# Kernel tuning notes

Measured on AMD Instinct MI355X. Metric: run time of the kernel, lower is better.

## Reference

```python
import jax, jax.numpy as jnp
import numpy as np

B, N, D, W = 4, 4096, 256, 7
K = 2 * W + 1  # 15 taps: positions [i-2w, ..., i]
H = 4 * D
EPS = 1e-5


def layer_norm(x, g, b):
    mu = jnp.mean(x, axis=-1, keepdims=True)
    var = jnp.mean(jnp.square(x - mu), axis=-1, keepdims=True)
    return (x - mu) * jax.lax.rsqrt(var + EPS) * g + b


def setup_inputs() -> dict:
    key = jax.random.key(0)
    ks = jax.random.split(key, 8)
    s = 0.02
    return {
        "x": jax.random.normal(ks[0], (B, N, D), dtype=jnp.float32),
        # w_mix[k] is the DxD block of the (K*D -> D) Linear acting on offset k-2w
        "w_mix": (jax.random.normal(ks[1], (K, D, D), dtype=jnp.float32) * s),
        "b_mix": jnp.zeros((D,), dtype=jnp.float32),
        "g1": jnp.ones((D,), jnp.float32) + 0.1 * jax.random.normal(ks[2], (D,), jnp.float32),
        "b1": 0.1 * jax.random.normal(ks[3], (D,), jnp.float32),
        "w_ff1": jax.random.normal(ks[4], (D, H), dtype=jnp.float32) * s,
        "b_ff1": jnp.zeros((H,), dtype=jnp.float32),
        "w_ff2": jax.random.normal(ks[5], (H, D), dtype=jnp.float32) * s,
        "b_ff2": jnp.zeros((D,), dtype=jnp.float32),
        "g2": jnp.ones((D,), jnp.float32) + 0.1 * jax.random.normal(ks[6], (D,), jnp.float32),
        "b2": 0.1 * jax.random.normal(ks[7], (D,), jnp.float32),
    }


def reference(x, w_mix, b_mix, g1, b1, w_ff1, b_ff1, w_ff2, b_ff2, g2, b2):
    # Causal windowed concat + Linear == causal 1D conv with kernel K=2w+1.
    # torch feats chunk k holds x[i - 2w + k]; conv tap k with left pad 2w
    # sees exactly x[i - 2w + k], so kernel = mix weight reshaped (K, D, D).
    mix = jax.lax.conv_general_dilated(
        x, w_mix, window_strides=(1,), padding=[(2 * W, 0)],
        dimension_numbers=("NWC", "WIO", "NWC"),
    ) + b_mix  # [B, N, D]
    # Dropout is identity in eval mode (reference baseline).
    h = layer_norm(x + mix, g1, b1)
    ff = jnp.dot(jax.nn.gelu(jnp.dot(h, w_ff1) + b_ff1, approximate=False), w_ff2) + b_ff2
    return layer_norm(h + ff, g2, b2)
```

## Files before the change

kernel.cpp:

```cpp
#include <hip/hip_runtime.h>
#include <cstdint>

#define DD     256
#define HH     1024
#define NNSEQ  4096
#define KDIM   3840
#define NSTEPS 120
#define MT     64
#define XROWS  78
#define XPITCH 264
#define EPSLN  1e-5f

typedef unsigned short u16;
typedef __attribute__((ext_vector_type(8))) short short8;
typedef __attribute__((ext_vector_type(4))) float f32x4;

#define MFMA(a, b, c) __builtin_amdgcn_mfma_f32_16x16x32_bf16(a, b, c, 0, 0, 0)

__device__ __forceinline__ u16 f2bf(float f) {
  unsigned u = __float_as_uint(f);
  u += 0x7FFF + ((u >> 16) & 1);
  return (u16)(u >> 16);
}
__device__ __forceinline__ float bf2f(u16 s) { return __uint_as_float(((unsigned)s) << 16); }

__global__ __launch_bounds__(256) void k_prep(
    const float* __restrict__ wmix, const float* __restrict__ wff1,
    const float* __restrict__ wff2, u16* __restrict__ wpk,
    u16* __restrict__ w1pk, u16* __restrict__ w2pk)
{
  __shared__ float t[32][257];
  const int b = blockIdx.x, tid = threadIdx.x;

  u16* dst;
  if (b < 120) {
    dst = wpk + (size_t)b * 8192;
    for (int r = 0; r < 32; ++r)
      t[r][tid] = wmix[(size_t)(b * 32 + r) * 256 + tid];
  } else if (b < 152) {
    const int u = b - 120, c = u >> 3, s = u & 7;
    dst = w1pk + (size_t)u * 8192;
    for (int r = 0; r < 32; ++r)
      t[r][tid] = wff1[(size_t)(s * 32 + r) * 1024 + c * 256 + tid];
  } else {
    const int u = b - 152, c = u >> 3, s = u & 7;
    dst = w2pk + (size_t)u * 8192;
    for (int r = 0; r < 32; ++r)
      t[r][tid] = wff2[(size_t)(c * 256 + s * 32 + r) * 256 + tid];
  }
  __syncthreads();

  const int l = tid & 63, q = l >> 4, cl = l & 15;
#pragma unroll
  for (int f = 0; f < 4; ++f) {
    const int fi = f * 4 + (tid >> 6);
    const int n = fi * 16 + cl;
    uint4 pk;
    unsigned* p = (unsigned*)&pk;
#pragma unroll
    for (int jj = 0; jj < 4; ++jj)
      p[jj] = (unsigned)f2bf(t[q * 8 + jj * 2][n]) | ((unsigned)f2bf(t[q * 8 + jj * 2 + 1][n]) << 16);
    *(uint4*)&dst[(size_t)fi * 512 + l * 8] = pk;
  }
}

__global__ __launch_bounds__(512, 2) void k_fused(
    const float* __restrict__ x, const u16* __restrict__ wpk,
    const float* __restrict__ bmix, const float* __restrict__ g1,
    const float* __restrict__ b1, const u16* __restrict__ w1pk,
    const float* __restrict__ bf1, const u16* __restrict__ w2pk,
    const float* __restrict__ bf2, const float* __restrict__ g2,
    const float* __restrict__ b2, float* __restrict__ out)
{
  __shared__ u16 smA[XROWS * XPITCH];
  __shared__ u16 asb[64 * XPITCH];
  __shared__ float redS[4][64], redS2[4][64];
  __shared__ float muL[64], invL[64];

  const int tid = threadIdx.x;
  const int wv = tid >> 6, l = tid & 63, q = l >> 4, cl = l & 15;
  const int mg = wv >> 2, ng = wv & 3;
  const long tok0 = (long)blockIdx.x * MT;
  const int n0 = (int)(tok0 & (NNSEQ - 1));

  {
    const int cslot = (tid & 63) * 4;
    for (int r = tid >> 6; r < XROWS; r += 8) {
      const int nloc = n0 - 14 + r;
      float4 v = make_float4(0.f, 0.f, 0.f, 0.f);
      if (nloc >= 0) v = *(const float4*)&x[(tok0 - 14 + r) * DD + cslot];
      uint2 pk;
      pk.x = (unsigned)f2bf(v.x) | ((unsigned)f2bf(v.y) << 16);
      pk.y = (unsigned)f2bf(v.z) | ((unsigned)f2bf(v.w) << 16);
      *(uint2*)&smA[r * XPITCH + cslot] = pk;
    }
  }
  __syncthreads();

  f32x4 acc[2][4];
#pragma unroll
  for (int nt = 0; nt < 4; ++nt) {
    const float bm = bmix[ng * 64 + nt * 16 + cl];
#pragma unroll
    for (int mt = 0; mt < 2; ++mt) acc[mt][nt] = (f32x4){bm, bm, bm, bm};
  }

  const u16* bbase = wpk + (size_t)ng * 2048 + (size_t)l * 8;

#define LOAD_A(dst, s_)                                                        \
  {                                                                            \
    const int xrow = (s_) >> 3, c0 = ((s_) & 7) * 32;                          \
    _Pragma("unroll")                                                          \
    for (int mt = 0; mt < 2; ++mt)                                             \
      dst[mt] = *(const short8*)&smA[(xrow + mg * 32 + mt * 16 + cl) * XPITCH + c0 + q * 8]; \
  }
#define LOAD_B(dst, s_)                                                        \
  {                                                                            \
    const u16* bp = bbase + (size_t)(s_) * 8192;                               \
    _Pragma("unroll")                                                          \
    for (int nt = 0; nt < 4; ++nt)                                             \
      dst[nt] = *(const short8*)(bp + nt * 512);                               \
  }

  {
    short8 af[3][2], bfr[3][4];
    LOAD_A(af[0], 0) LOAD_B(bfr[0], 0)
    LOAD_A(af[1], 1) LOAD_B(bfr[1], 1)
    LOAD_A(af[2], 2) LOAD_B(bfr[2], 2)

#pragma unroll 3
    for (int s = 0; s < NSTEPS; ++s) {
      const int cur = s % 3;
#pragma unroll
      for (int mt = 0; mt < 2; ++mt)
#pragma unroll
        for (int nt = 0; nt < 4; ++nt)
          acc[mt][nt] = MFMA(af[cur][mt], bfr[cur][nt], acc[mt][nt]);
      if (s + 3 < NSTEPS) {
        LOAD_A(af[cur], s + 3)
        LOAD_B(bfr[cur], s + 3)
      }
    }
  }
#undef LOAD_A
#undef LOAD_B

#pragma unroll
  for (int mt = 0; mt < 2; ++mt)
#pragma unroll
    for (int nt = 0; nt < 4; ++nt) {
      const int col = ng * 64 + nt * 16 + cl;
#pragma unroll
      for (int reg = 0; reg < 4; ++reg) {
        const int row = mg * 32 + mt * 16 + q * 4 + reg;
        acc[mt][nt][reg] += x[(tok0 + row) * DD + col];
      }
    }

  {
    float ps[2][4], ps2[2][4];
#pragma unroll
    for (int mt = 0; mt < 2; ++mt)
#pragma unroll
      for (int reg = 0; reg < 4; ++reg) {
        float s = 0.f, s2 = 0.f;
#pragma unroll
        for (int nt = 0; nt < 4; ++nt) { const float y = acc[mt][nt][reg]; s += y; s2 += y * y; }
#pragma unroll
        for (int off = 1; off < 16; off <<= 1) { s += __shfl_xor(s, off, 64); s2 += __shfl_xor(s2, off, 64); }
        ps[mt][reg] = s; ps2[mt][reg] = s2;
      }
    if (cl == 0) {
#pragma unroll
      for (int mt = 0; mt < 2; ++mt)
#pragma unroll
        for (int reg = 0; reg < 4; ++reg) {
          const int row = mg * 32 + mt * 16 + q * 4 + reg;
          redS[ng][row] = ps[mt][reg]; redS2[ng][row] = ps2[mt][reg];
        }
    }
  }
  __syncthreads();
  if (tid < 64) {
    const float s  = redS[0][tid] + redS[1][tid] + redS[2][tid] + redS[3][tid];
    const float s2 = redS2[0][tid] + redS2[1][tid] + redS2[2][tid] + redS2[3][tid];
    const float mu = s * (1.f / DD);
    const float var = s2 * (1.f / DD) - mu * mu;
    muL[tid] = mu; invL[tid] = rsqrtf(var + EPSLN);
  }
  __syncthreads();

#pragma unroll
  for (int nt = 0; nt < 4; ++nt) {
    const int col = ng * 64 + nt * 16 + cl;
    const float gv = g1[col], bv = b1[col];
#pragma unroll
    for (int mt = 0; mt < 2; ++mt)
#pragma unroll
      for (int reg = 0; reg < 4; ++reg) {
        const int row = mg * 32 + mt * 16 + q * 4 + reg;
        const float hv = (acc[mt][nt][reg] - muL[row]) * invL[row] * gv + bv;
        smA[row * XPITCH + col] = f2bf(hv);
      }
  }
  __syncthreads();

  f32x4 acc2[2][4];
#pragma unroll
  for (int nt = 0; nt < 4; ++nt) {
    const float bv = bf2[ng * 64 + nt * 16 + cl];
#pragma unroll
    for (int mt = 0; mt < 2; ++mt) acc2[mt][nt] = (f32x4){bv, bv, bv, bv};
  }

  for (int c = 0; c < 4; ++c) {
    f32x4 acc1[2][4];
#pragma unroll
    for (int nt = 0; nt < 4; ++nt) {
      const float bv = bf1[c * 256 + ng * 64 + nt * 16 + cl];
#pragma unroll
      for (int mt = 0; mt < 2; ++mt) acc1[mt][nt] = (f32x4){bv, bv, bv, bv};
    }
#pragma unroll
    for (int s = 0; s < 8; ++s) {
      short8 a[2], b[4];
#pragma unroll
      for (int mt = 0; mt < 2; ++mt)
        a[mt] = *(const short8*)&smA[(mg * 32 + mt * 16 + cl) * XPITCH + s * 32 + q * 8];
      const u16* bp = w1pk + (size_t)(c * 8 + s) * 8192 + ng * 2048 + (size_t)l * 8;
#pragma unroll
      for (int nt = 0; nt < 4; ++nt)
        b[nt] = *(const short8*)(bp + nt * 512);
#pragma unroll
      for (int mt = 0; mt < 2; ++mt)
#pragma unroll
        for (int nt = 0; nt < 4; ++nt)
          acc1[mt][nt] = MFMA(a[mt], b[nt], acc1[mt][nt]);
    }
#pragma unroll
    for (int mt = 0; mt < 2; ++mt)
#pragma unroll
      for (int nt = 0; nt < 4; ++nt)
#pragma unroll
        for (int reg = 0; reg < 4; ++reg) {
          const float v = acc1[mt][nt][reg];
          const float g = 0.5f * v * (1.f + erff(v * 0.70710678118654752f));
          asb[(mg * 32 + mt * 16 + q * 4 + reg) * XPITCH + ng * 64 + nt * 16 + cl] = f2bf(g);
        }
    __syncthreads();
#pragma unroll
    for (int s = 0; s < 8; ++s) {
      short8 a[2], b[4];
#pragma unroll
      for (int mt = 0; mt < 2; ++mt)
        a[mt] = *(const short8*)&asb[(mg * 32 + mt * 16 + cl) * XPITCH + s * 32 + q * 8];
      const u16* bp = w2pk + (size_t)(c * 8 + s) * 8192 + ng * 2048 + (size_t)l * 8;
#pragma unroll
      for (int nt = 0; nt < 4; ++nt)
        b[nt] = *(const short8*)(bp + nt * 512);
#pragma unroll
      for (int mt = 0; mt < 2; ++mt)
#pragma unroll
        for (int nt = 0; nt < 4; ++nt)
          acc2[mt][nt] = MFMA(a[mt], b[nt], acc2[mt][nt]);
    }
    __syncthreads();
  }

#pragma unroll
  for (int mt = 0; mt < 2; ++mt)
#pragma unroll
    for (int nt = 0; nt < 4; ++nt) {
      const int col = ng * 64 + nt * 16 + cl;
#pragma unroll
      for (int reg = 0; reg < 4; ++reg) {
        const int row = mg * 32 + mt * 16 + q * 4 + reg;
        acc2[mt][nt][reg] += bf2f(smA[row * XPITCH + col]);
      }
    }

  {
    float ps[2][4], ps2[2][4];
#pragma unroll
    for (int mt = 0; mt < 2; ++mt)
#pragma unroll
      for (int reg = 0; reg < 4; ++reg) {
        float s = 0.f, s2 = 0.f;
#pragma unroll
        for (int nt = 0; nt < 4; ++nt) { const float y = acc2[mt][nt][reg]; s += y; s2 += y * y; }
#pragma unroll
        for (int off = 1; off < 16; off <<= 1) { s += __shfl_xor(s, off, 64); s2 += __shfl_xor(s2, off, 64); }
        ps[mt][reg] = s; ps2[mt][reg] = s2;
      }
    if (cl == 0) {
#pragma unroll
      for (int mt = 0; mt < 2; ++mt)
#pragma unroll
        for (int reg = 0; reg < 4; ++reg) {
          const int row = mg * 32 + mt * 16 + q * 4 + reg;
          redS[ng][row] = ps[mt][reg]; redS2[ng][row] = ps2[mt][reg];
        }
    }
  }
  __syncthreads();
  if (tid < 64) {
    const float s  = redS[0][tid] + redS[1][tid] + redS[2][tid] + redS[3][tid];
    const float s2 = redS2[0][tid] + redS2[1][tid] + redS2[2][tid] + redS2[3][tid];
    const float mu = s * (1.f / DD);
    const float var = s2 * (1.f / DD) - mu * mu;
    muL[tid] = mu; invL[tid] = rsqrtf(var + EPSLN);
  }
  __syncthreads();

#pragma unroll
  for (int nt = 0; nt < 4; ++nt) {
    const int col = ng * 64 + nt * 16 + cl;
    const float gv = g2[col], bv = b2[col];
#pragma unroll
    for (int mt = 0; mt < 2; ++mt)
#pragma unroll
      for (int reg = 0; reg < 4; ++reg) {
        const int row = mg * 32 + mt * 16 + q * 4 + reg;
        out[(tok0 + row) * DD + col] = (acc2[mt][nt][reg] - muL[row]) * invL[row] * gv + bv;
      }
  }
}

extern "C" void kernel_launch(void* const* d_in, const int* in_sizes, int n_in,
                              void* d_out, int out_size, void* d_ws, size_t ws_size,
                              hipStream_t stream) {
  const float* x    = (const float*)d_in[0];
  const float* wmix = (const float*)d_in[1];
  const float* bmix = (const float*)d_in[2];
  const float* g1   = (const float*)d_in[3];
  const float* b1   = (const float*)d_in[4];
  const float* wff1 = (const float*)d_in[5];
  const float* bff1 = (const float*)d_in[6];
  const float* wff2 = (const float*)d_in[7];
  const float* bff2 = (const float*)d_in[8];
  const float* g2   = (const float*)d_in[9];
  const float* b2   = (const float*)d_in[10];
  float* out = (float*)d_out;

  u16* wpk  = (u16*)d_ws;
  u16* w1pk = wpk + 983040;
  u16* w2pk = w1pk + 262144;

  k_prep<<<184, 256, 0, stream>>>(wmix, wff1, wff2, wpk, w1pk, w2pk);

  const int R = 4 * NNSEQ;
  k_fused<<<R / MT, 512, 0, stream>>>(x, wpk, bmix, g1, b1,
                                      w1pk, bff1, w2pk, bff2, g2, b2, out);
}
```

Baseline: 168.1 us.

## Split fused kernel into conv and FFN kernels with split-K wave groups

```diff
diff --git a/kernel.cpp b/kernel.cpp
--- a/kernel.cpp
+++ b/kernel.cpp
@@ -5,10 +5,11 @@
 #define HH     1024
 #define NNSEQ  4096
 #define KDIM   3840
-#define NSTEPS 120
 #define MT     64
 #define XROWS  78
 #define XPITCH 264
+#define APITCH 520
+#define FPITCH 260
 #define EPSLN  1e-5f
 
 typedef unsigned short u16;
@@ -38,15 +39,15 @@
     for (int r = 0; r < 32; ++r)
       t[r][tid] = wmix[(size_t)(b * 32 + r) * 256 + tid];
   } else if (b < 152) {
-    const int u = b - 120, c = u >> 3, s = u & 7;
+    const int u = b - 120, c2 = u >> 3, s = u & 7;
     dst = w1pk + (size_t)u * 8192;
     for (int r = 0; r < 32; ++r)
-      t[r][tid] = wff1[(size_t)(s * 32 + r) * 1024 + c * 256 + tid];
+      t[r][tid] = wff1[(size_t)(s * 32 + r) * 1024 + c2 * 256 + tid];
   } else {
-    const int u = b - 152, c = u >> 3, s = u & 7;
+    const int u = b - 152, c2 = u >> 3, s = u & 7;
     dst = w2pk + (size_t)u * 8192;
     for (int r = 0; r < 32; ++r)
-      t[r][tid] = wff2[(size_t)(c * 256 + s * 32 + r) * 256 + tid];
+      t[r][tid] = wff2[(size_t)(c2 * 256 + s * 32 + r) * 256 + tid];
   }
   __syncthreads();
 
@@ -64,23 +65,17 @@
   }
 }
 
-__global__ __launch_bounds__(512, 2) void k_fused(
+__global__ __launch_bounds__(512) void k_conv(
     const float* __restrict__ x, const u16* __restrict__ wpk,
-    const float* __restrict__ bmix, const float* __restrict__ g1,
-    const float* __restrict__ b1, const u16* __restrict__ w1pk,
-    const float* __restrict__ bf1, const u16* __restrict__ w2pk,
-    const float* __restrict__ bf2, const float* __restrict__ g2,
-    const float* __restrict__ b2, float* __restrict__ out)
+    const float* __restrict__ bmix, u16* __restrict__ yb)
 {
-  __shared__ u16 smA[XROWS * XPITCH];
-  __shared__ u16 asb[64 * XPITCH];
-  __shared__ float redS[4][64], redS2[4][64];
-  __shared__ float muL[64], invL[64];
+  __shared__ u16 xs[XROWS * XPITCH];
 
   const int tid = threadIdx.x;
   const int wv = tid >> 6, l = tid & 63, q = l >> 4, cl = l & 15;
   const int mg = wv >> 2, ng = wv & 3;
-  const long tok0 = (long)blockIdx.x * MT;
+  const int mtile = blockIdx.x >> 2, nb = blockIdx.x & 3;
+  const long tok0 = (long)mtile * MT;
   const int n0 = (int)(tok0 & (NNSEQ - 1));
 
   {
@@ -92,90 +87,248 @@
       uint2 pk;
       pk.x = (unsigned)f2bf(v.x) | ((unsigned)f2bf(v.y) << 16);
       pk.y = (unsigned)f2bf(v.z) | ((unsigned)f2bf(v.w) << 16);
-      *(uint2*)&smA[r * XPITCH + cslot] = pk;
-    }
-  }
-  __syncthreads();
-
-  f32x4 acc[2][4];
-#pragma unroll
-  for (int nt = 0; nt < 4; ++nt) {
-    const float bm = bmix[ng * 64 + nt * 16 + cl];
-#pragma unroll
-    for (int mt = 0; mt < 2; ++mt) acc[mt][nt] = (f32x4){bm, bm, bm, bm};
-  }
-
-  const u16* bbase = wpk + (size_t)ng * 2048 + (size_t)l * 8;
-
-#define LOAD_A(dst, s_)                                                        \
-  {                                                                            \
-    const int xrow = (s_) >> 3, c0 = ((s_) & 7) * 32;                          \
-    _Pragma("unroll")                                                          \
-    for (int mt = 0; mt < 2; ++mt)                                             \
-      dst[mt] = *(const short8*)&smA[(xrow + mg * 32 + mt * 16 + cl) * XPITCH + c0 + q * 8]; \
-  }
-#define LOAD_B(dst, s_)                                                        \
-  {                                                                            \
-    const u16* bp = bbase + (size_t)(s_) * 8192;                               \
-    _Pragma("unroll")                                                          \
-    for (int nt = 0; nt < 4; ++nt)                                             \
-      dst[nt] = *(const short8*)(bp + nt * 512);                               \
-  }
-
-  {
-    short8 af[3][2], bfr[3][4];
+      *(uint2*)&xs[r * XPITCH + cslot] = pk;
+    }
+  }
+  __syncthreads();
+
+  f32x4 acc[4];
+  {
+    const float bm = (mg == 0) ? bmix[nb * 64 + ng * 16 + cl] : 0.f;
+#pragma unroll
+    for (int mt = 0; mt < 4; ++mt) acc[mt] = (f32x4){bm, bm, bm, bm};
+  }
+
+  const u16* bbase = wpk + (size_t)(mg * 60) * 8192 + (size_t)(nb * 4 + ng) * 512 + (size_t)l * 8;
+
+#define LOAD_A(dst, s_)                                                         \
+  {                                                                             \
+    const int ks = mg * 60 + (s_);                                              \
+    const int xrow = ks >> 3, c0 = (ks & 7) * 32;                               \
+    _Pragma("unroll")                                                           \
+    for (int mt = 0; mt < 4; ++mt)                                              \
+      dst[mt] = *(const short8*)&xs[(xrow + mt * 16 + cl) * XPITCH + c0 + q * 8]; \
+  }
+#define LOAD_B(dst, s_) dst = *(const short8*)(bbase + (size_t)(s_) * 8192);
+
+  {
+    short8 af[4][4], bfr[4];
     LOAD_A(af[0], 0) LOAD_B(bfr[0], 0)
     LOAD_A(af[1], 1) LOAD_B(bfr[1], 1)
     LOAD_A(af[2], 2) LOAD_B(bfr[2], 2)
-
-#pragma unroll 3
-    for (int s = 0; s < NSTEPS; ++s) {
-      const int cur = s % 3;
-#pragma unroll
-      for (int mt = 0; mt < 2; ++mt)
-#pragma unroll
-        for (int nt = 0; nt < 4; ++nt)
-          acc[mt][nt] = MFMA(af[cur][mt], bfr[cur][nt], acc[mt][nt]);
-      if (s + 3 < NSTEPS) {
-        LOAD_A(af[cur], s + 3)
-        LOAD_B(bfr[cur], s + 3)
+    LOAD_A(af[3], 3) LOAD_B(bfr[3], 3)
+
+#pragma unroll 4
+    for (int s = 0; s < 60; ++s) {
+      const int cur = s & 3;
+#pragma unroll
+      for (int mt = 0; mt < 4; ++mt)
+        acc[mt] = MFMA(af[cur][mt], bfr[cur], acc[mt]);
+      if (s + 4 < 60) {
+        LOAD_A(af[cur], s + 4)
+        LOAD_B(bfr[cur], s + 4)
       }
     }
   }
 #undef LOAD_A
 #undef LOAD_B
 
-#pragma unroll
-  for (int mt = 0; mt < 2; ++mt)
+  __syncthreads();
+  float* rbuf = (float*)xs;
+  if (mg == 1) {
+#pragma unroll
+    for (int mt = 0; mt < 4; ++mt)
+#pragma unroll
+      for (int reg = 0; reg < 4; ++reg)
+        rbuf[(mt * 16 + q * 4 + reg) * 65 + ng * 16 + cl] = acc[mt][reg];
+  }
+  __syncthreads();
+
+  if (mg == 0) {
+#pragma unroll
+    for (int mt = 0; mt < 4; ++mt)
+#pragma unroll
+      for (int reg = 0; reg < 4; ++reg) {
+        const int row = mt * 16 + q * 4 + reg;
+        const int col = nb * 64 + ng * 16 + cl;
+        const float y = acc[mt][reg] + rbuf[row * 65 + ng * 16 + cl]
+                      + x[(tok0 + row) * DD + col];
+        yb[(tok0 + row) * DD + col] = f2bf(y);
+      }
+  }
+}
+
+__global__ __launch_bounds__(512) void k_ffn(
+    const u16* __restrict__ yb, const float* __restrict__ g1,
+    const float* __restrict__ b1, const u16* __restrict__ w1pk,
+    const float* __restrict__ bf1, const u16* __restrict__ w2pk,
+    const float* __restrict__ bf2, const float* __restrict__ g2,
+    const float* __restrict__ b2, float* __restrict__ out)
+{
+  __shared__ u16 hs[64 * XPITCH];
+  __shared__ u16 asb[64 * APITCH];
+  __shared__ float redS[4][64], redS2[4][64];
+  __shared__ float muL[64], invL[64];
+
+  const int tid = threadIdx.x;
+  const int wv = tid >> 6, l = tid & 63, q = l >> 4, cl = l & 15;
+  const int mg = wv >> 2, ng = wv & 3;
+  const long tok0 = (long)blockIdx.x * MT;
+
+  {
+    const int chunk = tid & 31;
+#pragma unroll
+    for (int i = 0; i < 4; ++i) {
+      const int row = (tid >> 5) + i * 16;
+      *(uint4*)&hs[row * XPITCH + chunk * 8] = *(const uint4*)&yb[(tok0 + row) * DD + chunk * 8];
+    }
+  }
+  __syncthreads();
+
+  {
+    const int row = tid >> 3, seg = tid & 7;
+    uint4 v[4];
+#pragma unroll
+    for (int i = 0; i < 4; ++i)
+      v[i] = *(const uint4*)&hs[row * XPITCH + seg * 32 + i * 8];
+    float yv[32];
+#pragma unroll
+    for (int i = 0; i < 4; ++i) {
+      const unsigned* w = (const unsigned*)&v[i];
+#pragma unroll
+      for (int j = 0; j < 4; ++j) {
+        yv[i * 8 + j * 2]     = __uint_as_float(w[j] << 16);
+        yv[i * 8 + j * 2 + 1] = __uint_as_float(w[j] & 0xffff0000u);
+      }
+    }
+    float s = 0.f, s2 = 0.f;
+#pragma unroll
+    for (int k = 0; k < 32; ++k) { s += yv[k]; s2 += yv[k] * yv[k]; }
+#pragma unroll
+    for (int off = 1; off < 8; off <<= 1) { s += __shfl_xor(s, off, 64); s2 += __shfl_xor(s2, off, 64); }
+    const float mu  = s * (1.f / DD);
+    const float var = s2 * (1.f / DD) - mu * mu;
+    const float inv = rsqrtf(var + EPSLN);
+#pragma unroll
+    for (int i = 0; i < 4; ++i) {
+      const float4 gv0 = *(const float4*)&g1[seg * 32 + i * 8];
+      const float4 gv1 = *(const float4*)&g1[seg * 32 + i * 8 + 4];
+      const float4 bv0 = *(const float4*)&b1[seg * 32 + i * 8];
+      const float4 bv1 = *(const float4*)&b1[seg * 32 + i * 8 + 4];
+      const float g[8] = {gv0.x, gv0.y, gv0.z, gv0.w, gv1.x, gv1.y, gv1.z, gv1.w};
+      const float bb[8] = {bv0.x, bv0.y, bv0.z, bv0.w, bv1.x, bv1.y, bv1.z, bv1.w};
+      uint4 pk;
+      unsigned* p = (unsigned*)&pk;
+#pragma unroll
+      for (int j = 0; j < 4; ++j) {
+        const float h0 = (yv[i * 8 + j * 2]     - mu) * inv * g[j * 2]     + bb[j * 2];
+        const float h1 = (yv[i * 8 + j * 2 + 1] - mu) * inv * g[j * 2 + 1] + bb[j * 2 + 1];
+        p[j] = (unsigned)f2bf(h0) | ((unsigned)f2bf(h1) << 16);
+      }
+      *(uint4*)&hs[row * XPITCH + seg * 32 + i * 8] = pk;
+    }
+  }
+  __syncthreads();
+
+  f32x4 acc2[4][4];
+#pragma unroll
+  for (int nt = 0; nt < 4; ++nt) {
+    const float bv = (mg == 0) ? bf2[ng * 64 + nt * 16 + cl] : 0.f;
+#pragma unroll
+    for (int mt = 0; mt < 4; ++mt) acc2[mt][nt] = (f32x4){bv, bv, bv, bv};
+  }
+
+  for (int c = 0; c < 2; ++c) {
+    f32x4 acc1[4][4];
 #pragma unroll
     for (int nt = 0; nt < 4; ++nt) {
-      const int col = ng * 64 + nt * 16 + cl;
+      const float bv = bf1[c * 512 + wv * 64 + nt * 16 + cl];
+#pragma unroll
+      for (int mt = 0; mt < 4; ++mt) acc1[mt][nt] = (f32x4){bv, bv, bv, bv};
+    }
+#pragma unroll
+    for (int s = 0; s < 8; ++s) {
+      short8 a[4], b[4];
+#pragma unroll
+      for (int mt = 0; mt < 4; ++mt)
+        a[mt] = *(const short8*)&hs[(mt * 16 + cl) * XPITCH + s * 32 + q * 8];
+      const u16* bp = w1pk + (size_t)((c * 2 + mg) * 8 + s) * 8192 + (size_t)(ng * 4) * 512 + (size_t)l * 8;
+#pragma unroll
+      for (int nt = 0; nt < 4; ++nt)
+        b[nt] = *(const short8*)(bp + nt * 512);
+#pragma unroll
+      for (int mt = 0; mt < 4; ++mt)
+#pragma unroll
+        for (int nt = 0; nt < 4; ++nt)
+          acc1[mt][nt] = MFMA(a[mt], b[nt], acc1[mt][nt]);
+    }
+#pragma unroll
+    for (int mt = 0; mt < 4; ++mt)
+#pragma unroll
+      for (int nt = 0; nt < 4; ++nt)
+#pragma unroll
+        for (int reg = 0; reg < 4; ++reg) {
+          const float v = acc1[mt][nt][reg];
+          const float g = 0.5f * v * (1.f + erff(v * 0.70710678118654752f));
+          asb[(mt * 16 + q * 4 + reg) * APITCH + wv * 64 + nt * 16 + cl] = f2bf(g);
+        }
+    __syncthreads();
+#pragma unroll
+    for (int s = 0; s < 8; ++s) {
+      short8 a[4], b[4];
+#pragma unroll
+      for (int mt = 0; mt < 4; ++mt)
+        a[mt] = *(const short8*)&asb[(mt * 16 + cl) * APITCH + mg * 256 + s * 32 + q * 8];
+      const u16* bp = w2pk + (size_t)((c * 2 + mg) * 8 + s) * 8192 + (size_t)(ng * 4) * 512 + (size_t)l * 8;
+#pragma unroll
+      for (int nt = 0; nt < 4; ++nt)
+        b[nt] = *(const short8*)(bp + nt * 512);
+#pragma unroll
+      for (int mt = 0; mt < 4; ++mt)
+#pragma unroll
+        for (int nt = 0; nt < 4; ++nt)
+          acc2[mt][nt] = MFMA(a[mt], b[nt], acc2[mt][nt]);
+    }
+    __syncthreads();
+  }
+
+  float* fbuf = (float*)asb;
+  if (mg == 1) {
+#pragma unroll
+    for (int mt = 0; mt < 4; ++mt)
+#pragma unroll
+      for (int nt = 0; nt < 4; ++nt)
+#pragma unroll
+        for (int reg = 0; reg < 4; ++reg)
+          fbuf[(mt * 16 + q * 4 + reg) * FPITCH + ng * 64 + nt * 16 + cl] = acc2[mt][nt][reg];
+  }
+  __syncthreads();
+
+  if (mg == 0) {
+    float ps[4][4], ps2[4][4];
+#pragma unroll
+    for (int mt = 0; mt < 4; ++mt)
 #pragma unroll
       for (int reg = 0; reg < 4; ++reg) {
-        const int row = mg * 32 + mt * 16 + q * 4 + reg;
-        acc[mt][nt][reg] += x[(tok0 + row) * DD + col];
-      }
-    }
-
-  {
-    float ps[2][4], ps2[2][4];
-#pragma unroll
-    for (int mt = 0; mt < 2; ++mt)
-#pragma unroll
-      for (int reg = 0; reg < 4; ++reg) {
+        const int row = mt * 16 + q * 4 + reg;
         float s = 0.f, s2 = 0.f;
 #pragma unroll
-        for (int nt = 0; nt < 4; ++nt) { const float y = acc[mt][nt][reg]; s += y; s2 += y * y; }
+        for (int nt = 0; nt < 4; ++nt) {
+          const int col = ng * 64 + nt * 16 + cl;
+          float y = acc2[mt][nt][reg] + fbuf[row * FPITCH + col] + bf2f(hs[row * XPITCH + col]);
+          acc2[mt][nt][reg] = y;
+          s += y; s2 += y * y;
+        }
 #pragma unroll
         for (int off = 1; off < 16; off <<= 1) { s += __shfl_xor(s, off, 64); s2 += __shfl_xor(s2, off, 64); }
         ps[mt][reg] = s; ps2[mt][reg] = s2;
       }
     if (cl == 0) {
 #pragma unroll
-      for (int mt = 0; mt < 2; ++mt)
+      for (int mt = 0; mt < 4; ++mt)
 #pragma unroll
         for (int reg = 0; reg < 4; ++reg) {
-          const int row = mg * 32 + mt * 16 + q * 4 + reg;
+          const int row = mt * 16 + q * 4 + reg;
           redS[ng][row] = ps[mt][reg]; redS2[ng][row] = ps2[mt][reg];
         }
     }
@@ -190,139 +343,19 @@
   }
   __syncthreads();
 
-#pragma unroll
-  for (int nt = 0; nt < 4; ++nt) {
-    const int col = ng * 64 + nt * 16 + cl;
-    const float gv = g1[col], bv = b1[col];
-#pragma unroll
-    for (int mt = 0; mt < 2; ++mt)
-#pragma unroll
-      for (int reg = 0; reg < 4; ++reg) {
-        const int row = mg * 32 + mt * 16 + q * 4 + reg;
-        const float hv = (acc[mt][nt][reg] - muL[row]) * invL[row] * gv + bv;
-        smA[row * XPITCH + col] = f2bf(hv);
-      }
-  }
-  __syncthreads();
-
-  f32x4 acc2[2][4];
-#pragma unroll
-  for (int nt = 0; nt < 4; ++nt) {
-    const float bv = bf2[ng * 64 + nt * 16 + cl];
-#pragma unroll
-    for (int mt = 0; mt < 2; ++mt) acc2[mt][nt] = (f32x4){bv, bv, bv, bv};
-  }
-
-  for (int c = 0; c < 4; ++c) {
-    f32x4 acc1[2][4];
-#pragma unroll
-    for (int nt = 0; nt < 4; ++nt) {
-      const float bv = bf1[c * 256 + ng * 64 + nt * 16 + cl];
-#pragma unroll
-      for (int mt = 0; mt < 2; ++mt) acc1[mt][nt] = (f32x4){bv, bv, bv, bv};
-    }
-#pragma unroll
-    for (int s = 0; s < 8; ++s) {
-      short8 a[2], b[4];
-#pragma unroll
-      for (int mt = 0; mt < 2; ++mt)
-        a[mt] = *(const short8*)&smA[(mg * 32 + mt * 16 + cl) * XPITCH + s * 32 + q * 8];
-      const u16* bp = w1pk + (size_t)(c * 8 + s) * 8192 + ng * 2048 + (size_t)l * 8;
-#pragma unroll
-      for (int nt = 0; nt < 4; ++nt)
-        b[nt] = *(const short8*)(bp + nt * 512);
-#pragma unroll
-      for (int mt = 0; mt < 2; ++mt)
-#pragma unroll
-        for (int nt = 0; nt < 4; ++nt)
-          acc1[mt][nt] = MFMA(a[mt], b[nt], acc1[mt][nt]);
-    }
-#pragma unroll
-    for (int mt = 0; mt < 2; ++mt)
-#pragma unroll
-      for (int nt = 0; nt < 4; ++nt)
-#pragma unroll
-        for (int reg = 0; reg < 4; ++reg) {
-          const float v = acc1[mt][nt][reg];
-          const float g = 0.5f * v * (1.f + erff(v * 0.70710678118654752f));
-          asb[(mg * 32 + mt * 16 + q * 4 + reg) * XPITCH + ng * 64 + nt * 16 + cl] = f2bf(g);
-        }
-    __syncthreads();
-#pragma unroll
-    for (int s = 0; s < 8; ++s) {
-      short8 a[2], b[4];
-#pragma unroll
-      for (int mt = 0; mt < 2; ++mt)
-        a[mt] = *(const short8*)&asb[(mg * 32 + mt * 16 + cl) * XPITCH + s * 32 + q * 8];
-      const u16* bp = w2pk + (size_t)(c * 8 + s) * 8192 + ng * 2048 + (size_t)l * 8;
-#pragma unroll
-      for (int nt = 0; nt < 4; ++nt)
-        b[nt] = *(const short8*)(bp + nt * 512);
-#pragma unroll
-      for (int mt = 0; mt < 2; ++mt)
-#pragma unroll
-        for (int nt = 0; nt < 4; ++nt)
-          acc2[mt][nt] = MFMA(a[mt], b[nt], acc2[mt][nt]);
-    }
-    __syncthreads();
-  }
-
-#pragma unroll
-  for (int mt = 0; mt < 2; ++mt)
+  if (mg == 0) {
 #pragma unroll
     for (int nt = 0; nt < 4; ++nt) {
       const int col = ng * 64 + nt * 16 + cl;
-#pragma unroll
-      for (int reg = 0; reg < 4; ++reg) {
-        const int row = mg * 32 + mt * 16 + q * 4 + reg;
-        acc2[mt][nt][reg] += bf2f(smA[row * XPITCH + col]);
-      }
-    }
-
-  {
-    float ps[2][4], ps2[2][4];
-#pragma unroll
-    for (int mt = 0; mt < 2; ++mt)
-#pragma unroll
-      for (int reg = 0; reg < 4; ++reg) {
-        float s = 0.f, s2 = 0.f;
-#pragma unroll
-        for (int nt = 0; nt < 4; ++nt) { const float y = acc2[mt][nt][reg]; s += y; s2 += y * y; }
-#pragma unroll
-        for (int off = 1; off < 16; off <<= 1) { s += __shfl_xor(s, off, 64); s2 += __shfl_xor(s2, off, 64); }
-        ps[mt][reg] = s; ps2[mt][reg] = s2;
-      }
-    if (cl == 0) {
-#pragma unroll
-      for (int mt = 0; mt < 2; ++mt)
+      const float gv = g2[col], bv = b2[col];
+#pragma unroll
+      for (int mt = 0; mt < 4; ++mt)
 #pragma unroll
         for (int reg = 0; reg < 4; ++reg) {
-          const int row = mg * 32 + mt * 16 + q * 4 + reg;
-          redS[ng][row] = ps[mt][reg]; redS2[ng][row] = ps2[mt][reg];
+          const int row = mt * 16 + q * 4 + reg;
+          out[(tok0 + row) * DD + col] = (acc2[mt][nt][reg] - muL[row]) * invL[row] * gv + bv;
         }
     }
-  }
-  __syncthreads();
-  if (tid < 64) {
-    const float s  = redS[0][tid] + redS[1][tid] + redS[2][tid] + redS[3][tid];
-    const float s2 = redS2[0][tid] + redS2[1][tid] + redS2[2][tid] + redS2[3][tid];
-    const float mu = s * (1.f / DD);
-    const float var = s2 * (1.f / DD) - mu * mu;
-    muL[tid] = mu; invL[tid] = rsqrtf(var + EPSLN);
-  }
-  __syncthreads();
-
-#pragma unroll
-  for (int nt = 0; nt < 4; ++nt) {
-    const int col = ng * 64 + nt * 16 + cl;
-    const float gv = g2[col], bv = b2[col];
-#pragma unroll
-    for (int mt = 0; mt < 2; ++mt)
-#pragma unroll
-      for (int reg = 0; reg < 4; ++reg) {
-        const int row = mg * 32 + mt * 16 + q * 4 + reg;
-        out[(tok0 + row) * DD + col] = (acc2[mt][nt][reg] - muL[row]) * invL[row] * gv + bv;
-      }
   }
 }
 
@@ -345,10 +378,10 @@
   u16* wpk  = (u16*)d_ws;
   u16* w1pk = wpk + 983040;
   u16* w2pk = w1pk + 262144;
+  u16* yb   = w2pk + 262144;
 
   k_prep<<<184, 256, 0, stream>>>(wmix, wff1, wff2, wpk, w1pk, w2pk);
 
-  const int R = 4 * NNSEQ;
-  k_fused<<<R / MT, 512, 0, stream>>>(x, wpk, bmix, g1, b1,
-                                      w1pk, bff1, w2pk, bff2, g2, b2, out);
-}
+  k_conv<<<1024, 512, 0, stream>>>(x, wpk, bmix, yb);
+  k_ffn <<<256, 512, 0, stream>>>(yb, g1, b1, w1pk, bff1, w2pk, bff2, g2, b2, out);
+}
```

New measurement: 165.6 us. No clear change (-1.5%).

## Split conv GEMM K-dimension across wave groups with LDS reduction

Applied to the files above, without the earlier changes.

```diff
diff --git a/kernel.cpp b/kernel.cpp
--- a/kernel.cpp
+++ b/kernel.cpp
@@ -5,10 +5,10 @@
 #define HH     1024
 #define NNSEQ  4096
 #define KDIM   3840
-#define NSTEPS 120
 #define MT     64
 #define XROWS  78
 #define XPITCH 264
+#define SLOTP  260
 #define EPSLN  1e-5f
 
 typedef unsigned short u16;
@@ -38,15 +38,15 @@
     for (int r = 0; r < 32; ++r)
       t[r][tid] = wmix[(size_t)(b * 32 + r) * 256 + tid];
   } else if (b < 152) {
-    const int u = b - 120, c = u >> 3, s = u & 7;
+    const int u = b - 120, c2 = u >> 3, s = u & 7;
     dst = w1pk + (size_t)u * 8192;
     for (int r = 0; r < 32; ++r)
-      t[r][tid] = wff1[(size_t)(s * 32 + r) * 1024 + c * 256 + tid];
+      t[r][tid] = wff1[(size_t)(s * 32 + r) * 1024 + c2 * 256 + tid];
   } else {
-    const int u = b - 152, c = u >> 3, s = u & 7;
+    const int u = b - 152, c2 = u >> 3, s = u & 7;
     dst = w2pk + (size_t)u * 8192;
     for (int r = 0; r < 32; ++r)
-      t[r][tid] = wff2[(size_t)(c * 256 + s * 32 + r) * 256 + tid];
+      t[r][tid] = wff2[(size_t)(c2 * 256 + s * 32 + r) * 256 + tid];
   }
   __syncthreads();
 
@@ -64,7 +64,7 @@
   }
 }
 
-__global__ __launch_bounds__(512, 2) void k_fused(
+__global__ __launch_bounds__(512) void k_fused(
     const float* __restrict__ x, const u16* __restrict__ wpk,
     const float* __restrict__ bmix, const float* __restrict__ g1,
     const float* __restrict__ b1, const u16* __restrict__ w1pk,
@@ -72,8 +72,8 @@
     const float* __restrict__ bf2, const float* __restrict__ g2,
     const float* __restrict__ b2, float* __restrict__ out)
 {
-  __shared__ u16 smA[XROWS * XPITCH];
-  __shared__ u16 asb[64 * XPITCH];
+  __shared__ u16 bufA[XROWS * XPITCH];
+  __shared__ float bufB[64 * SLOTP];
   __shared__ float redS[4][64], redS2[4][64];
   __shared__ float muL[64], invL[64];
 
@@ -92,51 +92,52 @@
       uint2 pk;
       pk.x = (unsigned)f2bf(v.x) | ((unsigned)f2bf(v.y) << 16);
       pk.y = (unsigned)f2bf(v.z) | ((unsigned)f2bf(v.w) << 16);
-      *(uint2*)&smA[r * XPITCH + cslot] = pk;
-    }
-  }
-  __syncthreads();
-
-  f32x4 acc[2][4];
+      *(uint2*)&bufA[r * XPITCH + cslot] = pk;
+    }
+  }
+  __syncthreads();
+
+  f32x4 acc[4][4];
 #pragma unroll
   for (int nt = 0; nt < 4; ++nt) {
-    const float bm = bmix[ng * 64 + nt * 16 + cl];
-#pragma unroll
-    for (int mt = 0; mt < 2; ++mt) acc[mt][nt] = (f32x4){bm, bm, bm, bm};
-  }
-
-  const u16* bbase = wpk + (size_t)ng * 2048 + (size_t)l * 8;
-
-#define LOAD_A(dst, s_)                                                        \
-  {                                                                            \
-    const int xrow = (s_) >> 3, c0 = ((s_) & 7) * 32;                          \
-    _Pragma("unroll")                                                          \
-    for (int mt = 0; mt < 2; ++mt)                                             \
-      dst[mt] = *(const short8*)&smA[(xrow + mg * 32 + mt * 16 + cl) * XPITCH + c0 + q * 8]; \
-  }
-#define LOAD_B(dst, s_)                                                        \
-  {                                                                            \
-    const u16* bp = bbase + (size_t)(s_) * 8192;                               \
-    _Pragma("unroll")                                                          \
-    for (int nt = 0; nt < 4; ++nt)                                             \
-      dst[nt] = *(const short8*)(bp + nt * 512);                               \
+    const float bm = (mg == 0) ? bmix[ng * 64 + nt * 16 + cl] : 0.f;
+#pragma unroll
+    for (int mt = 0; mt < 4; ++mt) acc[mt][nt] = (f32x4){bm, bm, bm, bm};
+  }
+
+  const u16* bbase = wpk + (size_t)(mg * 60) * 8192 + (size_t)(ng * 4) * 512 + (size_t)l * 8;
+
+#define LOAD_A(dst, s_)                                                         \
+  {                                                                             \
+    const int ks = mg * 60 + (s_);                                              \
+    const int xrow = ks >> 3, c0 = (ks & 7) * 32;                               \
+    _Pragma("unroll")                                                           \
+    for (int mt = 0; mt < 4; ++mt)                                              \
+      dst[mt] = *(const short8*)&bufA[(xrow + mt * 16 + cl) * XPITCH + c0 + q * 8]; \
+  }
+#define LOAD_B(dst, s_)                                                         \
+  {                                                                             \
+    const u16* bp = bbase + (size_t)(s_) * 8192;                                \
+    _Pragma("unroll")                                                           \
+    for (int nt = 0; nt < 4; ++nt)                                              \
+      dst[nt] = *(const short8*)(bp + nt * 512);                                \
   }
 
   {
-    short8 af[3][2], bfr[3][4];
+    short8 af[3][4], bfr[3][4];
     LOAD_A(af[0], 0) LOAD_B(bfr[0], 0)
     LOAD_A(af[1], 1) LOAD_B(bfr[1], 1)
     LOAD_A(af[2], 2) LOAD_B(bfr[2], 2)
 
 #pragma unroll 3
-    for (int s = 0; s < NSTEPS; ++s) {
+    for (int s = 0; s < 60; ++s) {
       const int cur = s % 3;
 #pragma unroll
-      for (int mt = 0; mt < 2; ++mt)
+      for (int mt = 0; mt < 4; ++mt)
 #pragma unroll
         for (int nt = 0; nt < 4; ++nt)
           acc[mt][nt] = MFMA(af[cur][mt], bfr[cur][nt], acc[mt][nt]);
-      if (s + 3 < NSTEPS) {
+      if (s + 3 < 60) {
         LOAD_A(af[cur], s + 3)
         LOAD_B(bfr[cur], s + 3)
       }
@@ -145,37 +146,44 @@
 #undef LOAD_A
 #undef LOAD_B
 
-#pragma unroll
-  for (int mt = 0; mt < 2; ++mt)
-#pragma unroll
-    for (int nt = 0; nt < 4; ++nt) {
-      const int col = ng * 64 + nt * 16 + cl;
+  __syncthreads();
+  if (mg == 1) {
+#pragma unroll
+    for (int mt = 0; mt < 4; ++mt)
+#pragma unroll
+      for (int nt = 0; nt < 4; ++nt)
+#pragma unroll
+        for (int reg = 0; reg < 4; ++reg)
+          bufB[(mt * 16 + q * 4 + reg) * SLOTP + ng * 64 + nt * 16 + cl] = acc[mt][nt][reg];
+  }
+  __syncthreads();
+
+  if (mg == 0) {
+    float ps[4][4], ps2[4][4];
+#pragma unroll
+    for (int mt = 0; mt < 4; ++mt)
 #pragma unroll
       for (int reg = 0; reg < 4; ++reg) {
-        const int row = mg * 32 + mt * 16 + q * 4 + reg;
-        acc[mt][nt][reg] += x[(tok0 + row) * DD + col];
-      }
-    }
-
-  {
-    float ps[2][4], ps2[2][4];
-#pragma unroll
-    for (int mt = 0; mt < 2; ++mt)
-#pragma unroll
-      for (int reg = 0; reg < 4; ++reg) {
+        const int row = mt * 16 + q * 4 + reg;
         float s = 0.f, s2 = 0.f;
 #pragma unroll
-        for (int nt = 0; nt < 4; ++nt) { const float y = acc[mt][nt][reg]; s += y; s2 += y * y; }
+        for (int nt = 0; nt < 4; ++nt) {
+          const int col = ng * 64 + nt * 16 + cl;
+          const float y = acc[mt][nt][reg] + bufB[row * SLOTP + col]
+                        + x[(tok0 + row) * DD + col];
+          acc[mt][nt][reg] = y;
+          s += y; s2 += y * y;
+        }
 #pragma unroll
         for (int off = 1; off < 16; off <<= 1) { s += __shfl_xor(s, off, 64); s2 += __shfl_xor(s2, off, 64); }
         ps[mt][reg] = s; ps2[mt][reg] = s2;
       }
     if (cl == 0) {
 #pragma unroll
-      for (int mt = 0; mt < 2; ++mt)
+      for (int mt = 0; mt < 4; ++mt)
 #pragma unroll
         for (int reg = 0; reg < 4; ++reg) {
-          const int row = mg * 32 + mt * 16 + q * 4 + reg;
+          const int row = mt * 16 + q * 4 + reg;
           redS[ng][row] = ps[mt][reg]; redS2[ng][row] = ps2[mt][reg];
         }
     }
@@ -190,21 +198,24 @@
   }
   __syncthreads();
 
-#pragma unroll
-  for (int nt = 0; nt < 4; ++nt) {
-    const int col = ng * 64 + nt * 16 + cl;
-    const float gv = g1[col], bv = b1[col];
-#pragma unroll
-    for (int mt = 0; mt < 2; ++mt)
-#pragma unroll
-      for (int reg = 0; reg < 4; ++reg) {
-        const int row = mg * 32 + mt * 16 + q * 4 + reg;
-        const float hv = (acc[mt][nt][reg] - muL[row]) * invL[row] * gv + bv;
-        smA[row * XPITCH + col] = f2bf(hv);
-      }
-  }
-  __syncthreads();
-
+  if (mg == 0) {
+#pragma unroll
+    for (int nt = 0; nt < 4; ++nt) {
+      const int col = ng * 64 + nt * 16 + cl;
+      const float gv = g1[col], bv = b1[col];
+#pragma unroll
+      for (int mt = 0; mt < 4; ++mt)
+#pragma unroll
+        for (int reg = 0; reg < 4; ++reg) {
+          const int row = mt * 16 + q * 4 + reg;
+          const float hv = (acc[mt][nt][reg] - muL[row]) * invL[row] * gv + bv;
+          bufA[row * XPITCH + col] = f2bf(hv);
+        }
+    }
+  }
+  __syncthreads();
+
+  u16* asb = (u16*)bufB;
   f32x4 acc2[2][4];
 #pragma unroll
   for (int nt = 0; nt < 4; ++nt) {
@@ -226,8 +237,8 @@
       short8 a[2], b[4];
 #pragma unroll
       for (int mt = 0; mt < 2; ++mt)
-        a[mt] = *(const short8*)&smA[(mg * 32 + mt * 16 + cl) * XPITCH + s * 32 + q * 8];
-      const u16* bp = w1pk + (size_t)(c * 8 + s) * 8192 + ng * 2048 + (size_t)l * 8;
+        a[mt] = *(const short8*)&bufA[(mg * 32 + mt * 16 + cl) * XPITCH + s * 32 + q * 8];
+      const u16* bp = w1pk + (size_t)(c * 8 + s) * 8192 + (size_t)(ng * 4) * 512 + (size_t)l * 8;
 #pragma unroll
       for (int nt = 0; nt < 4; ++nt)
         b[nt] = *(const short8*)(bp + nt * 512);
@@ -254,7 +265,7 @@
 #pragma unroll
       for (int mt = 0; mt < 2; ++mt)
         a[mt] = *(const short8*)&asb[(mg * 32 + mt * 16 + cl) * XPITCH + s * 32 + q * 8];
-      const u16* bp = w2pk + (size_t)(c * 8 + s) * 8192 + ng * 2048 + (size_t)l * 8;
+      const u16* bp = w2pk + (size_t)(c * 8 + s) * 8192 + (size_t)(ng * 4) * 512 + (size_t)l * 8;
 #pragma unroll
       for (int nt = 0; nt < 4; ++nt)
         b[nt] = *(const short8*)(bp + nt * 512);
@@ -267,27 +278,21 @@
     __syncthreads();
   }
 
-#pragma unroll
-  for (int mt = 0; mt < 2; ++mt)
-#pragma unroll
-    for (int nt = 0; nt < 4; ++nt) {
-      const int col = ng * 64 + nt * 16 + cl;
+  {
+    float ps[2][4], ps2[2][4];
+#pragma unroll
+    for (int mt = 0; mt < 2; ++mt)
 #pragma unroll
       for (int reg = 0; reg < 4; ++reg) {
         const int row = mg * 32 + mt * 16 + q * 4 + reg;
-        acc2[mt][nt][reg] += bf2f(smA[row * XPITCH + col]);
-      }
-    }
-
-  {
-    float ps[2][4], ps2[2][4];
-#pragma unroll
-    for (int mt = 0; mt < 2; ++mt)
-#pragma unroll
-      for (int reg = 0; reg < 4; ++reg) {
         float s = 0.f, s2 = 0.f;
 #pragma unroll
-        for (int nt = 0; nt < 4; ++nt) { const float y = acc2[mt][nt][reg]; s += y; s2 += y * y; }
+        for (int nt = 0; nt < 4; ++nt) {
+          const int col = ng * 64 + nt * 16 + cl;
+          const float y = acc2[mt][nt][reg] + bf2f(bufA[row * XPITCH + col]);
+          acc2[mt][nt][reg] = y;
+          s += y; s2 += y * y;
+        }
 #pragma unroll
         for (int off = 1; off < 16; off <<= 1) { s += __shfl_xor(s, off, 64); s2 += __shfl_xor(s2, off, 64); }
         ps[mt][reg] = s; ps2[mt][reg] = s2;
@@ -348,7 +353,6 @@
 
   k_prep<<<184, 256, 0, stream>>>(wmix, wff1, wff2, wpk, w1pk, w2pk);
 
-  const int R = 4 * NNSEQ;
-  k_fused<<<R / MT, 512, 0, stream>>>(x, wpk, bmix, g1, b1,
-                                      w1pk, bff1, w2pk, bff2, g2, b2, out);
+  k_fused<<<256, 512, 0, stream>>>(x, wpk, bmix, g1, b1,
+                                   w1pk, bff1, w2pk, bff2, g2, b2, out);
 }
```

Result: faster. 160.3 us (-4.7%).
